# Kernel optimization log

Hardware: AMD Instinct MI355X
Metric: run time of the kernel (lower is better)

## Reference

```python
import jax, jax.numpy as jnp
import numpy as np

N_SAMPLES = 16384
SR = 22050.0
B = 8
N_OSC = 128
TWO_PI = 2.0 * np.pi


def setup_inputs() -> dict:
    key = jax.random.key(0)
    k1, k2, k3, k4 = jax.random.split(key, 4)
    centers = jnp.asarray(np.geomspace(20.0, 10000.0, N_OSC), dtype=jnp.float32)
    bandwidths = 0.108 * centers + 24.7  # erb(f)
    freq_params = jax.random.uniform(k1, (B, N_OSC, 64), jnp.float32, -10.0, 10.0)
    amp_params = jax.random.uniform(k2, (B, N_OSC, 64), jnp.float32, 0.0, 0.01)
    noise_params = jax.random.uniform(k3, (B, 17, 1024), jnp.float32, 0.0, 0.01)
    noise = jax.random.uniform(k4, (B, N_SAMPLES), jnp.float32, -1.0, 1.0)
    return {
        'freq_params': freq_params,
        'amp_params': amp_params,
        'noise_params': noise_params,
        'centers': centers,
        'bandwidths': bandwidths,
        'noise': noise,
    }


def linear_upsample(x, out_size):
    # F.upsample(mode='linear', align_corners=False) on last dim
    in_size = x.shape[-1]
    scale = in_size / out_size
    coords = (jnp.arange(out_size, dtype=jnp.float32) + 0.5) * scale - 0.5
    coords = jnp.clip(coords, 0.0, in_size - 1)
    lo = jnp.floor(coords).astype(jnp.int32)
    hi = jnp.minimum(lo + 1, in_size - 1)
    w = coords - lo.astype(jnp.float32)
    return x[..., lo] * (1.0 - w) + x[..., hi] * w


def oscillator_bank(frequency, amplitude, sample_rate):
    # frequency, amplitude: (batch, n_osc, n_samples)
    frequency = jnp.clip(frequency, 1.0, sample_rate / 2.0)
    omegas = frequency * (TWO_PI / sample_rate)
    phases = jnp.cumsum(omegas, axis=-1)  # phase accumulation (prefix scan)
    return jnp.sum(jnp.cos(phases) * amplitude, axis=1)  # (batch, n_samples)


def noise_bank2(x, noise):
    # x: (b, n_coeffs=17, n_frames=1024) filter magnitudes; noise: (b, total_samples)
    b, mags, frames = x.shape
    win = (mags - 1) * 2  # 32
    hop = win // 2        # 16
    total = hop * frames  # 16384
    npad = jnp.pad(noise, ((0, 0), (0, hop)))
    idx = jnp.arange(frames)[:, None] * hop + jnp.arange(win)[None, :]
    nf = npad[:, idx]
    coeffs = jnp.fft.rfft(nf, norm='ortho')            # (b, frames, mags) complex
    filtered = coeffs * jnp.transpose(x, (0, 2, 1))    # per-frame spectral shaping
    wav = jnp.fft.irfft(filtered, n=win, norm='ortho')
    a = wav[..., :hop]
    c = wav[..., hop:]
    c = jnp.concatenate([jnp.zeros_like(c[:, :1]), c[:, :-1]], axis=1)
    return (a + c).reshape(b, 1, total)


def reference(freq_params, amp_params, noise_params, centers, bandwidths, noise):
    orig_freq = jnp.tanh(freq_params)                                   # (B,128,64)
    freq = centers[None, :, None] + orig_freq * (bandwidths[None, :, None] / 2.0)
    orig_amp = jax.nn.relu(amp_params)                                  # (B,128,64)
    noisep = jax.nn.relu(noise_params)                                  # (B,17,1024)
    freq_up = linear_upsample(freq, N_SAMPLES)                          # (B,128,16384)
    amp_up = linear_upsample(orig_amp, N_SAMPLES)                       # (B,128,16384)
    x = oscillator_bank(freq_up, amp_up, SR)                            # (B,16384)
    n = noise_bank2(noisep, noise)                                      # (B,1,16384)
    x = x.reshape(n.shape)
    return (x + n, orig_freq, orig_amp, x, n)
```

## Files before the change

kernel.cpp:

```cpp
#include <hip/hip_runtime.h>
#include <math.h>

#define NS    16384
#define NOSC  128
#define NCTRL 64
#define NB    8

#define OFF_SUM 0
#define OFF_OF  131072
#define OFF_OA  196608
#define OFF_X   262144
#define OFF_N   393216

#define OMEGA_SC 2.8495170054464554e-4f

#define SEG_N      ((size_t)NB * 65 * NOSC)
#define SEG_FLOATS (5 * SEG_N)

__device__ __forceinline__ bool looks_like_freq(const float* __restrict__ A)
{
    float mx = 0.0f;
#pragma unroll
    for (int j = 0; j < 8; ++j) mx = fmaxf(mx, fabsf(A[j]));
    return mx > 0.02f;
}

__global__ __launch_bounds__(256) void k_prep(const float* __restrict__ pA,
                                              const float* __restrict__ pB,
                                              const float* __restrict__ cA,
                                              const float* __restrict__ cB,
                                              float* __restrict__ ws,
                                              float* __restrict__ out)
{
    const bool Afreq = looks_like_freq(pA);
    const float* fp = Afreq ? pA : pB;
    const float* ap = Afreq ? pB : pA;
    const bool AisC = (cA[0] < 23.0f);
    const float* centers = AisC ? cA : cB;
    const float* bws     = AisC ? cB : cA;

    float* __restrict__ sW  = ws;
    float* __restrict__ sDW = ws + SEG_N;
    float* __restrict__ sP  = ws + 2 * SEG_N;
    float* __restrict__ sA  = ws + 3 * SEG_N;
    float* __restrict__ sDA = ws + 4 * SEG_N;

    const int wid  = (blockIdx.x * 256 + threadIdx.x) >> 6;
    const int lane = threadIdx.x & 63;
    const int osc  = wid & (NOSC - 1);
    const int b    = wid >> 7;

    const float fv = fp[wid * NCTRL + lane];
    const float av = ap[wid * NCTRL + lane];
    const float of = tanhf(fv);
    const float ar = fmaxf(av, 0.0f);
    out[OFF_OF + wid * NCTRL + lane] = of;
    out[OFF_OA + wid * NCTRL + lane] = ar;

    float fr = fmaf(of, 0.5f * bws[osc], centers[osc]);
    fr = fminf(fmaxf(fr, 1.0f), 11025.0f);
    const float wk = fr * OMEGA_SC;

    const float wkm1 = __shfl_up(wk, 1, 64);
    double s = (lane == 0) ? 128.0 * (double)wk
                           : 128.0 * ((double)wkm1 + (double)wk);
#pragma unroll
    for (int d = 1; d < 64; d <<= 1) {
        double t = __shfl_up(s, d, 64);
        if (lane >= d) s += t;
    }
    const double TWOPI  = 6.283185307179586;
    const double INV2PI = 0.15915494309189535;
    const float Pk = (float)(s - TWOPI * rint(s * INV2PI));

    const float wk1 = __shfl_down(wk, 1, 64);
    const float ak1 = __shfl_down(ar, 1, 64);
    const float dw = (lane == 63) ? 0.0f : wk1 - wk;
    const float da = (lane == 63) ? 0.0f : ak1 - ar;

    const size_t idx = ((size_t)b * 65 + (lane + 1)) * NOSC + osc;
    sW[idx] = wk;  sDW[idx] = dw;  sP[idx] = Pk;  sA[idx] = ar;  sDA[idx] = da;
    if (lane == 0) {
        const size_t h = (size_t)b * 65 * NOSC + osc;
        sW[h] = wk;  sDW[h] = 0.0f;  sP[h] = 0.0f;  sA[h] = ar;  sDA[h] = 0.0f;
    }
}

__global__ __launch_bounds__(256) void k_fused(const float* __restrict__ ws,
                                               const float* __restrict__ nparams,
                                               const float* __restrict__ noise,
                                               float* __restrict__ out)
{
    const int T = blockIdx.x;
    const int b = blockIdx.y;
    const int tid = threadIdx.x;

    __shared__ float4 sQ[2][NOSC];
    __shared__ float  sD[2][NOSC];
    __shared__ float  nf[288];
    __shared__ float  cosT[32], sinT[32];
    __shared__ float  Rm[17][18], Sm[17][18];
    __shared__ float  y[17][33];

    {
        const int sgi = tid >> 7;
        const int o   = tid & 127;
        const size_t idx = ((size_t)b * 65 + T + sgi) * NOSC + o;
        const float* __restrict__ W  = ws;
        const float* __restrict__ DW = ws + SEG_N;
        const float* __restrict__ P  = ws + 2 * SEG_N;
        const float* __restrict__ A  = ws + 3 * SEG_N;
        const float* __restrict__ DA = ws + 4 * SEG_N;
        sQ[sgi][o] = make_float4(W[idx], DW[idx], P[idx], A[idx]);
        sD[sgi][o] = DA[idx];
    }

    if (tid < 32) {
        float th = (float)tid * 0.19634954084936207f;
        cosT[tid] = cosf(th);
        sinT[tid] = sinf(th);
    }
    const int sbase = T * 256 - 16;
    for (int j = tid; j < 288; j += 256) {
        int g = sbase + j;
        nf[j] = (g >= 0 && g < NS) ? noise[b * NS + g] : 0.0f;
    }
    __syncthreads();

    for (int w = tid; w < 289; w += 256) {
        int fi = (int)(((unsigned)w * 0x0F0F1u) >> 20);
        int k  = w - fi * 17;
        int f  = T * 16 + fi - 1;
        float re = 0.0f, im = 0.0f;
        const int s0 = fi * 16;
#pragma unroll
        for (int s = 0; s < 32; ++s) {
            float v = nf[s0 + s];
            int j = (k * s) & 31;
            re = fmaf(v, cosT[j], re);
            im = fmaf(v, sinT[j], im);
        }
        float m = (f >= 0) ? fmaxf(nparams[(b * 17 + k) * 1024 + f], 0.0f) : 0.0f;
        Rm[fi][k] = re * m;
        Sm[fi][k] = im * m;
    }
    __syncthreads();

    for (int w = tid; w < 544; w += 256) {
        int fi = w >> 5, t = w & 31;
        float a = Rm[fi][0];
#pragma unroll
        for (int k = 1; k <= 15; ++k) {
            int j = (k * t) & 31;
            a = fmaf(2.0f * Rm[fi][k], cosT[j], a);
            a = fmaf(2.0f * Sm[fi][k], sinT[j], a);
        }
        a += (t & 1) ? -Rm[fi][16] : Rm[fi][16];
        y[fi][t] = a * 0.03125f;
    }
    __syncthreads();

    const int hi = tid >> 7;
    const int r  = hi ? (tid - 128) : (tid + 128);
    float r1 = (float)(r + 1);
    if (T == 0 && hi == 0) r1 = (float)(tid + 1);
    const float r2 = (float)((r + 1) * (r + 1)) * (1.0f / 512.0f);
    const float fr = ((float)r + 0.5f) * (1.0f / 256.0f);

    float acc0 = 0.0f, acc1 = 0.0f, acc2 = 0.0f, acc3 = 0.0f;
#pragma unroll 4
    for (int o = 0; o < NOSC; o += 4) {
        float4 q0 = sQ[hi][o + 0];
        float4 q1 = sQ[hi][o + 1];
        float4 q2 = sQ[hi][o + 2];
        float4 q3 = sQ[hi][o + 3];
        float p0 = fmaf(r2, q0.y, fmaf(r1, q0.x, q0.z));
        float p1 = fmaf(r2, q1.y, fmaf(r1, q1.x, q1.z));
        float p2 = fmaf(r2, q2.y, fmaf(r1, q2.x, q2.z));
        float p3 = fmaf(r2, q3.y, fmaf(r1, q3.x, q3.z));
        float m0 = fmaf(fr, sD[hi][o + 0], q0.w);
        float m1 = fmaf(fr, sD[hi][o + 1], q1.w);
        float m2 = fmaf(fr, sD[hi][o + 2], q2.w);
        float m3 = fmaf(fr, sD[hi][o + 3], q3.w);
        acc0 = fmaf(__cosf(p0), m0, acc0);
        acc1 = fmaf(__cosf(p1), m1, acc1);
        acc2 = fmaf(__cosf(p2), m2, acc2);
        acc3 = fmaf(__cosf(p3), m3, acc3);
    }
    const float xv = (acc0 + acc1) + (acc2 + acc3);

    const int fo = tid >> 4, u = tid & 15;
    const float nv = y[fo + 1][u] + y[fo][16 + u];
    const int base = b * NS + T * 256 + tid;
    out[OFF_X   + base] = xv;
    out[OFF_N   + base] = nv;
    out[OFF_SUM + base] = xv + nv;
}

__global__ __launch_bounds__(256) void k_params(const float* __restrict__ pA,
                                                const float* __restrict__ pB,
                                                float* __restrict__ out)
{
    const bool Afreq = looks_like_freq(pA);
    const float* fp = Afreq ? pA : pB;
    const float* ap = Afreq ? pB : pA;
    int i = blockIdx.x * 256 + threadIdx.x;
    if (i < NB * NOSC * NCTRL) {
        out[OFF_OF + i] = tanhf(fp[i]);
        out[OFF_OA + i] = fmaxf(ap[i], 0.0f);
    }
}

__global__ __launch_bounds__(256) void k_osc_fb(const float* __restrict__ pA,
                                                const float* __restrict__ pB,
                                                const float* __restrict__ cA,
                                                const float* __restrict__ cB,
                                                float* __restrict__ out)
{
    const bool Afreq = looks_like_freq(pA);
    const float* fp = Afreq ? pA : pB;
    const float* ap = Afreq ? pB : pA;
    const bool AisC = (cA[0] < 23.0f);
    const float* centers = AisC ? cA : cB;
    const float* bws     = AisC ? cB : cA;

    const int T = blockIdx.x, b = blockIdx.y, tid = threadIdx.x;
    __shared__ float4 sQ[2][NOSC];
    __shared__ float  sD[2][NOSC];

    if (tid < NOSC) {
        const int gid = b * NOSC + tid;
        const int cm1 = (T == 0) ? 0 : T - 1;
        const int cp1 = (T == 63) ? 63 : T + 1;
        const float ctr = centers[tid];
        const float hbw = 0.5f * bws[tid];
        const float* f = fp + gid * NCTRL;
        const double TWOPI  = 6.283185307179586;
        const double INV2PI = 0.15915494309189535;
        double P = 0.0;
        float wprev = 0.0f, w_m1 = 0.0f, w_0 = 0.0f, w_p1 = 0.0f;
        float P_m1 = 0.0f, P_0 = 0.0f;
        const int kmax = (T == 63) ? 63 : T + 1;
        for (int k = 0; k <= kmax; ++k) {
            float of = tanhf(f[k]);
            float fr2 = fminf(fmaxf(fmaf(of, hbw, ctr), 1.0f), 11025.0f);
            float wk = fr2 * OMEGA_SC;
            if (k == 0) P = 128.0 * (double)wk;
            else        P += 128.0 * ((double)wprev + (double)wk);
            if (k == T - 1) { w_m1 = wk; P_m1 = (float)(P - TWOPI * rint(P * INV2PI)); }
            if (k == T)     { w_0  = wk; P_0  = (float)(P - TWOPI * rint(P * INV2PI)); }
            if (k == kmax)  { w_p1 = wk; }
            wprev = wk;
        }
        if (T == 0) { w_m1 = w_0; P_m1 = 0.0f; }
        const float* a = ap + gid * NCTRL;
        float a_m1 = fmaxf(a[cm1], 0.0f);
        float a_0  = fmaxf(a[T],   0.0f);
        float a_p1 = fmaxf(a[cp1], 0.0f);
        sQ[0][tid] = make_float4(w_m1, w_0 - w_m1, P_m1, a_m1);
        sD[0][tid] = a_0 - a_m1;
        sQ[1][tid] = make_float4(w_0, w_p1 - w_0, P_0, a_0);
        sD[1][tid] = a_p1 - a_0;
    }
    __syncthreads();

    const int hi = tid >> 7;
    const int r  = hi ? (tid - 128) : (tid + 128);
    float r1 = (float)(r + 1);
    if (T == 0 && hi == 0) r1 = (float)(tid + 1);
    const float r2 = (float)((r + 1) * (r + 1)) * (1.0f / 512.0f);
    const float fr = ((float)r + 0.5f) * (1.0f / 256.0f);

    float acc = 0.0f;
#pragma unroll 4
    for (int o = 0; o < NOSC; ++o) {
        float4 q = sQ[hi][o];
        float ph = fmaf(r1, q.x, q.z);
        ph       = fmaf(r2, q.y, ph);
        float amp = fmaf(fr, sD[hi][o], q.w);
        acc = fmaf(__cosf(ph), amp, acc);
    }
    out[OFF_X + b * NS + T * 256 + tid] = acc;
}

__global__ __launch_bounds__(544) void k_noise_fb(const float* __restrict__ nparams,
                                                  const float* __restrict__ noise,
                                                  float* __restrict__ out)
{
    __shared__ float nf[288];
    __shared__ float cosT[32], sinT[32];
    __shared__ float Rm[17][18], Sm[17][18];
    __shared__ float y[17][32];

    const int tid = threadIdx.x;
    const int b   = blockIdx.y;
    const int F0  = blockIdx.x * 16;
    const int fi  = tid >> 5;
    const int t   = tid & 31;
    const int f   = F0 + fi - 1;

    if (tid < 32) {
        float th = (float)tid * 0.19634954084936207f;
        cosT[tid] = cosf(th);
        sinT[tid] = sinf(th);
    }
    const int sbase = (F0 - 1) * 16;
    for (int j = tid; j < 288; j += 544) {
        int gidx = sbase + j;
        nf[j] = (gidx >= 0 && gidx < NS) ? noise[b * NS + gidx] : 0.0f;
    }
    __syncthreads();

    if (t < 17) {
        const int k = t;
        float re = 0.0f, im = 0.0f;
        const int s0 = fi * 16;
#pragma unroll
        for (int s = 0; s < 32; ++s) {
            float v = nf[s0 + s];
            int j = (k * s) & 31;
            re = fmaf(v, cosT[j], re);
            im = fmaf(v, sinT[j], im);
        }
        float m = (f >= 0) ? fmaxf(nparams[(b * 17 + k) * 1024 + f], 0.0f) : 0.0f;
        Rm[fi][k] = re * m;
        Sm[fi][k] = im * m;
    }
    __syncthreads();

    {
        float a = Rm[fi][0];
#pragma unroll
        for (int k = 1; k <= 15; ++k) {
            int j = (k * t) & 31;
            a = fmaf(2.0f * Rm[fi][k], cosT[j], a);
            a = fmaf(2.0f * Sm[fi][k], sinT[j], a);
        }
        a += (t & 1) ? -Rm[fi][16] : Rm[fi][16];
        y[fi][t] = a * 0.03125f;
    }
    __syncthreads();

    if (fi >= 1 && t < 16) {
        const int base = b * NS + f * 16 + t;
        float nv = y[fi][t] + y[fi - 1][16 + t];
        out[OFF_N + base] = nv;
        out[OFF_SUM + base] = out[OFF_X + base] + nv;
    }
}

extern "C" void kernel_launch(void* const* d_in, const int* in_sizes, int n_in,
                              void* d_out, int out_size, void* d_ws, size_t ws_size,
                              hipStream_t stream)
{
    const float* s65536[2] = {nullptr, nullptr}; int n65 = 0;
    const float* s128[2]   = {nullptr, nullptr}; int n12 = 0;
    const float* nparams = nullptr;
    const float* noise   = nullptr;
    for (int i = 0; i < n_in; ++i) {
        const float* p = (const float*)d_in[i];
        switch (in_sizes[i]) {
            case 65536:  if (n65 < 2) s65536[n65++] = p; break;
            case 128:    if (n12 < 2) s128[n12++]   = p; break;
            case 139264: nparams = p; break;
            case 131072: noise   = p; break;
            default: break;
        }
    }
    float* out = (float*)d_out;

    if (ws_size >= SEG_FLOATS * sizeof(float)) {
        float* ws = (float*)d_ws;
        k_prep<<<256, 256, 0, stream>>>(s65536[0], s65536[1], s128[0], s128[1],
                                        ws, out);
        k_fused<<<dim3(64, 8), 256, 0, stream>>>(ws, nparams, noise, out);
    } else {
        k_params<<<256, 256, 0, stream>>>(s65536[0], s65536[1], out);
        k_osc_fb<<<dim3(64, 8), 256, 0, stream>>>(s65536[0], s65536[1],
                                                  s128[0], s128[1], out);
        k_noise_fb<<<dim3(64, 8), 544, 0, stream>>>(nparams, noise, out);
    }
}
```

Baseline: 77.42 us.

## Split fused kernel into segment-aligned oscillator kernel and separate noise kernel

Splits the fused oscillator+noise kernel into two launches. The oscillator kernel makes each wavefront own one control segment and compute four samples per thread, so each shared-memory parameter load is reused across four samples. The noise kernel then reads the oscillator output back from global memory to form the sum. This adds a kernel launch and an extra global read/write of the oscillator signal, and cuts the oscillator grid to 136 blocks, which may underfill the GPU.

```diff
diff --git a/kernel.cpp b/kernel.cpp
--- a/kernel.cpp
+++ b/kernel.cpp
@@ -86,8 +86,63 @@
     }
 }
 
-__global__ __launch_bounds__(256) void k_fused(const float* __restrict__ ws,
-                                               const float* __restrict__ nparams,
+__global__ __launch_bounds__(256) void k_oscseg(const float* __restrict__ ws,
+                                                float* __restrict__ out)
+{
+    const int bx = blockIdx.x;
+    const int b  = blockIdx.y;
+    const int tid = threadIdx.x;
+
+    __shared__ float4 sQ[4][NOSC];
+    __shared__ float  sD[4][NOSC];
+
+    const int jbase = bx * 4;
+    const int jn = (jbase + 4 <= 65) ? 4 : (65 - jbase);
+    const float* __restrict__ W  = ws;
+    const float* __restrict__ DW = ws + SEG_N;
+    const float* __restrict__ P  = ws + 2 * SEG_N;
+    const float* __restrict__ A  = ws + 3 * SEG_N;
+    const float* __restrict__ DA = ws + 4 * SEG_N;
+    const size_t base = ((size_t)b * 65 + jbase) * NOSC;
+    for (int e = tid; e < jn * NOSC; e += 256) {
+        sQ[e >> 7][e & 127] = make_float4(W[base + e], DW[base + e],
+                                          P[base + e], A[base + e]);
+        sD[e >> 7][e & 127] = DA[base + e];
+    }
+    __syncthreads();
+
+    const int w = tid >> 6;
+    const int j = jbase + w;
+    if (j >= 65) return;
+    const int lane = tid & 63;
+    const int nit   = (j == 0 || j == 64) ? 2 : 4;
+    const int gbase = (j == 0) ? 0 : (256 * j - 128);
+
+    float r1[4], r2[4], fq[4], acc[4];
+#pragma unroll
+    for (int i = 0; i < 4; ++i) {
+        const int r = lane + 64 * i;
+        r1[i] = (float)(r + 1);
+        r2[i] = (float)((r + 1) * (r + 1)) * (1.0f / 512.0f);
+        fq[i] = ((float)r + 0.5f) * (1.0f / 256.0f);
+        acc[i] = 0.0f;
+    }
+#pragma unroll 4
+    for (int o = 0; o < NOSC; ++o) {
+        const float4 q = sQ[w][o];
+        const float  d = sD[w][o];
+#pragma unroll
+        for (int i = 0; i < 4; ++i) {
+            float ph = fmaf(r2[i], q.y, fmaf(r1[i], q.x, q.z));
+            float m  = fmaf(fq[i], d, q.w);
+            acc[i] = fmaf(__cosf(ph), m, acc[i]);
+        }
+    }
+    for (int i = 0; i < nit; ++i)
+        out[OFF_X + b * NS + gbase + lane + 64 * i] = acc[i];
+}
+
+__global__ __launch_bounds__(256) void k_noise(const float* __restrict__ nparams,
                                                const float* __restrict__ noise,
                                                float* __restrict__ out)
 {
@@ -95,25 +150,10 @@
     const int b = blockIdx.y;
     const int tid = threadIdx.x;
 
-    __shared__ float4 sQ[2][NOSC];
-    __shared__ float  sD[2][NOSC];
-    __shared__ float  nf[288];
-    __shared__ float  cosT[32], sinT[32];
-    __shared__ float  Rm[17][18], Sm[17][18];
-    __shared__ float  y[17][33];
-
-    {
-        const int sgi = tid >> 7;
-        const int o   = tid & 127;
-        const size_t idx = ((size_t)b * 65 + T + sgi) * NOSC + o;
-        const float* __restrict__ W  = ws;
-        const float* __restrict__ DW = ws + SEG_N;
-        const float* __restrict__ P  = ws + 2 * SEG_N;
-        const float* __restrict__ A  = ws + 3 * SEG_N;
-        const float* __restrict__ DA = ws + 4 * SEG_N;
-        sQ[sgi][o] = make_float4(W[idx], DW[idx], P[idx], A[idx]);
-        sD[sgi][o] = DA[idx];
-    }
+    __shared__ float nf[288];
+    __shared__ float cosT[32], sinT[32];
+    __shared__ float Rm[17][18], Sm[17][18];
+    __shared__ float y[17][33];
 
     if (tid < 32) {
         float th = (float)tid * 0.19634954084936207f;
@@ -121,9 +161,9 @@
         sinT[tid] = sinf(th);
     }
     const int sbase = T * 256 - 16;
-    for (int j = tid; j < 288; j += 256) {
-        int g = sbase + j;
-        nf[j] = (g >= 0 && g < NS) ? noise[b * NS + g] : 0.0f;
+    for (int jj = tid; jj < 288; jj += 256) {
+        int g = sbase + jj;
+        nf[jj] = (g >= 0 && g < NS) ? noise[b * NS + g] : 0.0f;
     }
     __syncthreads();
 
@@ -136,9 +176,9 @@
 #pragma unroll
         for (int s = 0; s < 32; ++s) {
             float v = nf[s0 + s];
-            int j = (k * s) & 31;
-            re = fmaf(v, cosT[j], re);
-            im = fmaf(v, sinT[j], im);
+            int jx = (k * s) & 31;
+            re = fmaf(v, cosT[jx], re);
+            im = fmaf(v, sinT[jx], im);
         }
         float m = (f >= 0) ? fmaxf(nparams[(b * 17 + k) * 1024 + f], 0.0f) : 0.0f;
         Rm[fi][k] = re * m;
@@ -151,48 +191,19 @@
         float a = Rm[fi][0];
 #pragma unroll
         for (int k = 1; k <= 15; ++k) {
-            int j = (k * t) & 31;
-            a = fmaf(2.0f * Rm[fi][k], cosT[j], a);
-            a = fmaf(2.0f * Sm[fi][k], sinT[j], a);
+            int jx = (k * t) & 31;
+            a = fmaf(2.0f * Rm[fi][k], cosT[jx], a);
+            a = fmaf(2.0f * Sm[fi][k], sinT[jx], a);
         }
         a += (t & 1) ? -Rm[fi][16] : Rm[fi][16];
         y[fi][t] = a * 0.03125f;
     }
     __syncthreads();
-
-    const int hi = tid >> 7;
-    const int r  = hi ? (tid - 128) : (tid + 128);
-    float r1 = (float)(r + 1);
-    if (T == 0 && hi == 0) r1 = (float)(tid + 1);
-    const float r2 = (float)((r + 1) * (r + 1)) * (1.0f / 512.0f);
-    const float fr = ((float)r + 0.5f) * (1.0f / 256.0f);
-
-    float acc0 = 0.0f, acc1 = 0.0f, acc2 = 0.0f, acc3 = 0.0f;
-#pragma unroll 4
-    for (int o = 0; o < NOSC; o += 4) {
-        float4 q0 = sQ[hi][o + 0];
-        float4 q1 = sQ[hi][o + 1];
-        float4 q2 = sQ[hi][o + 2];
-        float4 q3 = sQ[hi][o + 3];
-        float p0 = fmaf(r2, q0.y, fmaf(r1, q0.x, q0.z));
-        float p1 = fmaf(r2, q1.y, fmaf(r1, q1.x, q1.z));
-        float p2 = fmaf(r2, q2.y, fmaf(r1, q2.x, q2.z));
-        float p3 = fmaf(r2, q3.y, fmaf(r1, q3.x, q3.z));
-        float m0 = fmaf(fr, sD[hi][o + 0], q0.w);
-        float m1 = fmaf(fr, sD[hi][o + 1], q1.w);
-        float m2 = fmaf(fr, sD[hi][o + 2], q2.w);
-        float m3 = fmaf(fr, sD[hi][o + 3], q3.w);
-        acc0 = fmaf(__cosf(p0), m0, acc0);
-        acc1 = fmaf(__cosf(p1), m1, acc1);
-        acc2 = fmaf(__cosf(p2), m2, acc2);
-        acc3 = fmaf(__cosf(p3), m3, acc3);
-    }
-    const float xv = (acc0 + acc1) + (acc2 + acc3);
 
     const int fo = tid >> 4, u = tid & 15;
     const float nv = y[fo + 1][u] + y[fo][16 + u];
     const int base = b * NS + T * 256 + tid;
-    out[OFF_X   + base] = xv;
+    const float xv = out[OFF_X + base];
     out[OFF_N   + base] = nv;
     out[OFF_SUM + base] = xv + nv;
 }
@@ -305,9 +316,9 @@
         sinT[tid] = sinf(th);
     }
     const int sbase = (F0 - 1) * 16;
-    for (int j = tid; j < 288; j += 544) {
-        int gidx = sbase + j;
-        nf[j] = (gidx >= 0 && gidx < NS) ? noise[b * NS + gidx] : 0.0f;
+    for (int jj = tid; jj < 288; jj += 544) {
+        int gidx = sbase + jj;
+        nf[jj] = (gidx >= 0 && gidx < NS) ? noise[b * NS + gidx] : 0.0f;
     }
     __syncthreads();
 
@@ -318,9 +329,9 @@
 #pragma unroll
         for (int s = 0; s < 32; ++s) {
             float v = nf[s0 + s];
-            int j = (k * s) & 31;
-            re = fmaf(v, cosT[j], re);
-            im = fmaf(v, sinT[j], im);
+            int jx = (k * s) & 31;
+            re = fmaf(v, cosT[jx], re);
+            im = fmaf(v, sinT[jx], im);
         }
         float m = (f >= 0) ? fmaxf(nparams[(b * 17 + k) * 1024 + f], 0.0f) : 0.0f;
         Rm[fi][k] = re * m;
@@ -332,9 +343,9 @@
         float a = Rm[fi][0];
 #pragma unroll
         for (int k = 1; k <= 15; ++k) {
-            int j = (k * t) & 31;
-            a = fmaf(2.0f * Rm[fi][k], cosT[j], a);
-            a = fmaf(2.0f * Sm[fi][k], sinT[j], a);
+            int jx = (k * t) & 31;
+            a = fmaf(2.0f * Rm[fi][k], cosT[jx], a);
+            a = fmaf(2.0f * Sm[fi][k], sinT[jx], a);
         }
         a += (t & 1) ? -Rm[fi][16] : Rm[fi][16];
         y[fi][t] = a * 0.03125f;
@@ -373,7 +384,8 @@
         float* ws = (float*)d_ws;
         k_prep<<<256, 256, 0, stream>>>(s65536[0], s65536[1], s128[0], s128[1],
                                         ws, out);
-        k_fused<<<dim3(64, 8), 256, 0, stream>>>(ws, nparams, noise, out);
+        k_oscseg<<<dim3(17, 8), 256, 0, stream>>>(ws, out);
+        k_noise<<<dim3(64, 8), 256, 0, stream>>>(nparams, noise, out);
     } else {
         k_params<<<256, 256, 0, stream>>>(s65536[0], s65536[1], out);
         k_osc_fb<<<dim3(64, 8), 256, 0, stream>>>(s65536[0], s65536[1],
```

New measurement: 83.61 us. 8.0% more time.
